# Kernel optimization log

Hardware: AMD Instinct MI355X
Metric: run time of the kernel (lower is better)

Reference implementation:

```python
import jax, jax.numpy as jnp
import numpy as np

B, S, D = 8, 4096, 64
NEG = 10000.0


def setup_inputs() -> dict:
    key = jax.random.key(0)
    k1, k2, k3, k4 = jax.random.split(key, 4)
    query = jax.random.normal(k1, (B, S, D), dtype=jnp.float32)
    k_ = jax.random.normal(k2, (B, S, D), dtype=jnp.float32)
    v_ = jax.random.normal(k3, (B, S, D), dtype=jnp.float32)
    # padding mask [B, Sk]: mostly valid, tail padded for some rows
    lens = jax.random.randint(k4, (B,), S // 2, S + 1)
    mask = jnp.arange(S)[None, :] < lens[:, None]
    return {"query": query, "key": k_, "value": v_, "mask": mask}


def reference(query, key, value, mask):
    d = query.shape[-1]
    scale = 1.0 / jnp.sqrt(jnp.asarray(d, dtype=query.dtype))
    # e: [B, Sq, Sk]
    e = jnp.einsum("bqd,bkd->bqk", query, key) * scale
    # causal (history_only) mask: key index > query index gets -10000
    q_idx = jnp.arange(query.shape[1])[:, None]
    k_idx = jnp.arange(key.shape[1])[None, :]
    e = e - NEG * (k_idx > q_idx).astype(e.dtype)[None, :, :]
    # padding mask [B, 1, Sk]
    e = e - NEG * (1.0 - mask.astype(e.dtype))[:, None, :]
    attention = jax.nn.softmax(e, axis=-1)
    return jnp.einsum("bqk,bkd->bqd", attention, value)
```

## Files before the change

kernel.cpp:

```cpp
#include <hip/hip_runtime.h>
#include <hip/hip_bf16.h>

#define B_N 8
#define S_N 4096
#define D_N 64
#define NQT 64
#define TILE_BYTES 8192
#define SLOT_BYTES 4352

typedef __attribute__((ext_vector_type(8))) short bf16x8;
typedef __attribute__((ext_vector_type(4))) float f32x4;
typedef __attribute__((ext_vector_type(16))) float f32x16;
typedef unsigned uint2v __attribute__((ext_vector_type(2)));
typedef unsigned uint4v __attribute__((ext_vector_type(4)));

__device__ __forceinline__ float fast_exp2(float x) {
#if __has_builtin(__builtin_amdgcn_exp2f)
  return __builtin_amdgcn_exp2f(x);
#else
  return exp2f(x);
#endif
}

__device__ __forceinline__ unsigned f2bf_u(float x) {
  __hip_bfloat16 h = __float2bfloat16(x);
  return (unsigned)__builtin_bit_cast(unsigned short, h);
}
__device__ __forceinline__ unsigned pack2(float a, float b) {
  return f2bf_u(a) | (f2bf_u(b) << 16);
}

__device__ __forceinline__ void pl32swap(unsigned& a, unsigned& b) {
#if __has_builtin(__builtin_amdgcn_permlane32_swap)
  uint2v r = __builtin_amdgcn_permlane32_swap(a, b, false, false);
  a = r[0];
  b = r[1];
#else
  asm volatile("v_permlane32_swap_b32 %0, %1" : "+v"(a), "+v"(b));
#endif
}
__device__ __forceinline__ float xhalf_sum(float x) {
  unsigned a = __builtin_bit_cast(unsigned, x), b = a;
  pl32swap(a, b);
  return __builtin_bit_cast(float, a) + __builtin_bit_cast(float, b);
}

__global__ void __launch_bounds__(256)
lens_kernel(const unsigned* __restrict__ mask, int* __restrict__ lens) {
  int b = blockIdx.x, tid = threadIdx.x;
  unsigned first = mask[0];
  int cnt = 0;
  if (first == 0x01010101u) {
    const unsigned char* m = ((const unsigned char*)mask) + (size_t)b * S_N;
    for (int i = tid; i < S_N; i += 256) cnt += (m[i] != 0);
  } else if (first == 0x3F800000u) {
    const float* m = ((const float*)mask) + (size_t)b * S_N;
    for (int i = tid; i < S_N; i += 256) cnt += (m[i] != 0.0f);
  } else {
    const int* m = ((const int*)mask) + (size_t)b * S_N;
    for (int i = tid; i < S_N; i += 256) cnt += (m[i] != 0);
  }
#pragma unroll
  for (int off = 32; off > 0; off >>= 1) cnt += __shfl_down(cnt, off);
  __shared__ int acc[4];
  if ((tid & 63) == 0) acc[tid >> 6] = cnt;
  __syncthreads();
  if (tid == 0) lens[b] = acc[0] + acc[1] + acc[2] + acc[3];
}

__global__ void __launch_bounds__(256)
prep_kernel(const float* __restrict__ K, const float* __restrict__ V,
            char* __restrict__ Ks, char* __restrict__ VTs) {
  __shared__ float vl[64][72];
  const int bt = blockIdx.x, tid = threadIdx.x;
  const float* Kt = K + (size_t)bt * 4096;
  const float* Vt = V + (size_t)bt * 4096;
  char* Ko = Ks + (size_t)bt * TILE_BYTES;
  char* Vo = VTs + (size_t)bt * TILE_BYTES;
#pragma unroll
  for (int i = 0; i < 2; ++i) {
    int c = tid + i * 256;
    int r = c >> 3, j = c & 7;
    f32x4 a = *(const f32x4*)(Kt + r * 64 + j * 8);
    f32x4 b4 = *(const f32x4*)(Kt + r * 64 + j * 8 + 4);
    union { bf16x8 v; unsigned u[4]; } pk;
    pk.u[0] = pack2(a[0], a[1]);   pk.u[1] = pack2(a[2], a[3]);
    pk.u[2] = pack2(b4[0], b4[1]); pk.u[3] = pack2(b4[2], b4[3]);
    *(bf16x8*)(Ko + ((r >> 5) * 4 + (j >> 1)) * 1024 + (j & 1) * 512 +
               (r & 31) * 16) = pk.v;
    f32x4 va = *(const f32x4*)(Vt + r * 64 + j * 8);
    f32x4 vb = *(const f32x4*)(Vt + r * 64 + j * 8 + 4);
#pragma unroll
    for (int e = 0; e < 4; ++e) vl[j * 8 + e][r] = va[e];
#pragma unroll
    for (int e = 0; e < 4; ++e) vl[j * 8 + 4 + e][r] = vb[e];
  }
  __syncthreads();
#pragma unroll
  for (int i = 0; i < 2; ++i) {
    int c = tid + i * 256;
    int d = c >> 3, j = c & 7;
    f32x4 fa = *(const f32x4*)(&vl[d][j * 8]);
    f32x4 fb = *(const f32x4*)(&vl[d][j * 8 + 4]);
    union { bf16x8 v; unsigned u[4]; } pk;
    pk.u[0] = pack2(fa[0], fa[1]); pk.u[1] = pack2(fa[2], fa[3]);
    pk.u[2] = pack2(fb[0], fb[1]); pk.u[3] = pack2(fb[2], fb[3]);
    *(bf16x8*)(Vo + ((d >> 5) * 4 + (j >> 1)) * 1024 + (j & 1) * 512 +
               (d & 31) * 16) = pk.v;
  }
}

__global__ void __launch_bounds__(256, 4)
attn_kernel(const float* __restrict__ Qg, const char* __restrict__ Ks,
            const char* __restrict__ VTs, const int* __restrict__ lens,
            float* __restrict__ Og, char* __restrict__ parts,
            int M, int U) {
  const int tid = threadIdx.x;
  const int lane = tid & 63;
  const int w = tid >> 6;
  const int bid = blockIdx.x;
  const int b = bid & 7;
  const int u2 = (bid >> 3) * 4 + w;
  const int ws = u2 & 1;
  const int u = (U - 1) - (u2 >> 1);
  int a = 0;
  while ((M * (a + 1) * (a + 2)) / 2 <= u) ++a;
  const int v = u - (M * a * (a + 1)) / 2;
  const int qt = a * M + v / (a + 1);
  const int s = v - (v / (a + 1)) * (a + 1);
  const int kq = a + 1;

  const int q0 = qt * 64;
  const int len = lens[b];
  int nt = (len + 63) >> 6;
  if (qt + 1 < nt) nt = qt + 1;
  const int beg = s * M;
  int cnt = nt - beg;
  if (cnt > M) cnt = M;
  if (cnt < 0) cnt = 0;

  const int q31 = lane & 31;
  const int h = lane >> 5;
  const int qg = q0 + ws * 32 + q31;

  const char* Kb = Ks + (size_t)(b * NQT) * TILE_BYTES;
  const char* Vb = VTs + (size_t)(b * NQT) * TILE_BYTES;

  constexpr float CS = 0.125f * 1.4426950408889634f;
  bf16x8 qf[4];
#pragma unroll
  for (int c = 0; c < 4; ++c) {
    const float* src = Qg + ((size_t)(b * S_N) + qg) * D_N + c * 16 + h * 8;
    f32x4 aa = *(const f32x4*)src;
    f32x4 b4 = *(const f32x4*)(src + 4);
    union { bf16x8 v; unsigned u[4]; } pk;
    pk.u[0] = pack2(aa[0] * CS, aa[1] * CS);
    pk.u[1] = pack2(aa[2] * CS, aa[3] * CS);
    pk.u[2] = pack2(b4[0] * CS, b4[1] * CS);
    pk.u[3] = pack2(b4[2] * CS, b4[3] * CS);
    qf[c] = pk.v;
  }

  f32x16 ot0 = {}, ot1 = {};
  float l = 0.0f;
  const int H = 2 * cnt;

  for (int hs = 0; hs < H; ++hs) {
    const int t = beg + (hs >> 1);
    const int half = hs & 1;

    bf16x8 kd[4], vd[4];
    const char* Kt = Kb + (size_t)t * TILE_BYTES + half * 4096 + lane * 16;
    const char* Vt = Vb + (size_t)t * TILE_BYTES + half * 2048 + lane * 16;
#pragma unroll
    for (int c = 0; c < 4; ++c) kd[c] = *(const bf16x8*)(Kt + c * 1024);
    vd[0] = *(const bf16x8*)(Vt);
    vd[1] = *(const bf16x8*)(Vt + 1024);
    vd[2] = *(const bf16x8*)(Vt + 4096);
    vd[3] = *(const bf16x8*)(Vt + 5120);

    f32x16 sv;
#pragma unroll
    for (int i = 0; i < 16; ++i) sv[i] = -8.0f;
    __builtin_amdgcn_s_setprio(1);
#pragma unroll
    for (int c = 0; c < 4; ++c)
      sv = __builtin_amdgcn_mfma_f32_32x32x16_bf16(kd[c], qf[c], sv, 0, 0, 0);
    __builtin_amdgcn_s_setprio(0);

    const int kb0 = t * 64 + half * 32;
    if (t == qt || t * 64 + 64 > len) {
#pragma unroll
      for (int g = 0; g < 4; ++g)
#pragma unroll
        for (int jj = 0; jj < 4; ++jj) {
          int kg = kb0 + 8 * g + 4 * h + jj;
          if (kg > qg || kg >= len) sv[g * 4 + jj] = -10000.0f;
        }
    }

    float ps0 = 0.f, ps1 = 0.f, ps2 = 0.f, ps3 = 0.f;
#pragma unroll
    for (int g = 0; g < 4; ++g) {
      sv[4 * g + 0] = fast_exp2(sv[4 * g + 0]); ps0 += sv[4 * g + 0];
      sv[4 * g + 1] = fast_exp2(sv[4 * g + 1]); ps1 += sv[4 * g + 1];
      sv[4 * g + 2] = fast_exp2(sv[4 * g + 2]); ps2 += sv[4 * g + 2];
      sv[4 * g + 3] = fast_exp2(sv[4 * g + 3]); ps3 += sv[4 * g + 3];
    }
    l += xhalf_sum((ps0 + ps1) + (ps2 + ps3));

    unsigned opk[4][2];
#pragma unroll
    for (int g = 0; g < 4; ++g) {
      opk[g][0] = pack2(sv[4 * g + 0], sv[4 * g + 1]);
      opk[g][1] = pack2(sv[4 * g + 2], sv[4 * g + 3]);
    }
    bf16x8 pb2[2];
#pragma unroll
    for (int c2 = 0; c2 < 2; ++c2) {
      const int g0 = 2 * c2, g1 = g0 + 1;
      unsigned a0 = opk[g0][0], b0 = opk[g1][0];
      unsigned a1 = opk[g0][1], b1 = opk[g1][1];
      pl32swap(a0, b0);
      pl32swap(a1, b1);
      union { bf16x8 v; unsigned u[4]; } pk;
      pk.u[0] = a0; pk.u[1] = a1; pk.u[2] = b0; pk.u[3] = b1;
      pb2[c2] = pk.v;
    }

    __builtin_amdgcn_s_setprio(1);
    ot0 = __builtin_amdgcn_mfma_f32_32x32x16_bf16(vd[0], pb2[0], ot0, 0, 0, 0);
    ot0 = __builtin_amdgcn_mfma_f32_32x32x16_bf16(vd[1], pb2[1], ot0, 0, 0, 0);
    ot1 = __builtin_amdgcn_mfma_f32_32x32x16_bf16(vd[2], pb2[0], ot1, 0, 0, 0);
    ot1 = __builtin_amdgcn_mfma_f32_32x32x16_bf16(vd[3], pb2[1], ot1, 0, 0, 0);
    __builtin_amdgcn_s_setprio(0);
  }

  if (kq == 1) {
    float linv = 1.0f / l;
    float* orow = Og + ((size_t)(b * S_N) + qg) * D_N;
#pragma unroll
    for (int g = 0; g < 4; ++g) {
      f32x4 oa = {ot0[4 * g + 0] * linv, ot0[4 * g + 1] * linv,
                  ot0[4 * g + 2] * linv, ot0[4 * g + 3] * linv};
      *(f32x4*)(orow + 8 * g + 4 * h) = oa;
      f32x4 ob = {ot1[4 * g + 0] * linv, ot1[4 * g + 1] * linv,
                  ot1[4 * g + 2] * linv, ot1[4 * g + 3] * linv};
      *(f32x4*)(orow + 32 + 8 * g + 4 * h) = ob;
    }
  } else {
    char* slot = parts + (((size_t)b * U + u) * 2 + ws) * SLOT_BYTES;
    unsigned wv[16];
#pragma unroll
    for (int jj = 0; jj < 8; ++jj) {
      wv[jj] = pack2(ot0[2 * jj], ot0[2 * jj + 1]);
      wv[8 + jj] = pack2(ot1[2 * jj], ot1[2 * jj + 1]);
    }
    uint4v* dst = (uint4v*)(slot + lane * 64);
#pragma unroll
    for (int q4 = 0; q4 < 4; ++q4)
      dst[q4] = (uint4v){wv[4 * q4], wv[4 * q4 + 1], wv[4 * q4 + 2], wv[4 * q4 + 3]};
    *(float*)(slot + 4096 + lane * 4) = l;
  }
}

__global__ void __launch_bounds__(128)
merge_kernel(const char* __restrict__ parts, float* __restrict__ Og,
             int M, int U) {
  const int bid = blockIdx.x;
  const int b = bid & 7, qt = bid >> 3;
  const int a = qt / M;
  const int kq = a + 1;
  if (kq == 1) return;
  const int tid = threadIdx.x;
  const int ws = tid >> 6;
  const int lane = tid & 63;
  const int base_u = (M * a * (a + 1)) / 2 + (qt - a * M) * (a + 1);

  float acc[32];
#pragma unroll
  for (int i = 0; i < 32; ++i) acc[i] = 0.0f;
  float L = 0.0f;
  for (int s2 = 0; s2 < kq; ++s2) {
    const char* slot =
        parts + (((size_t)b * U + base_u + s2) * 2 + ws) * SLOT_BYTES;
    const uint4v* src = (const uint4v*)(slot + lane * 64);
#pragma unroll
    for (int q4 = 0; q4 < 4; ++q4) {
      uint4v wv = src[q4];
#pragma unroll
      for (int e = 0; e < 4; ++e) {
        unsigned uw = wv[e];
        acc[2 * (4 * q4 + e)] += __builtin_bit_cast(float, uw << 16);
        acc[2 * (4 * q4 + e) + 1] += __builtin_bit_cast(float, uw & 0xFFFF0000u);
      }
    }
    L += *(const float*)(slot + 4096 + lane * 4);
  }
  float linv = 1.0f / L;
  const int q31 = lane & 31;
  const int h = lane >> 5;
  float* orow = Og + ((size_t)(b * S_N) + qt * 64 + ws * 32 + q31) * D_N;
#pragma unroll
  for (int dt = 0; dt < 2; ++dt)
#pragma unroll
    for (int g = 0; g < 4; ++g) {
      f32x4 w = {acc[dt * 16 + 4 * g + 0] * linv, acc[dt * 16 + 4 * g + 1] * linv,
                 acc[dt * 16 + 4 * g + 2] * linv, acc[dt * 16 + 4 * g + 3] * linv};
      *(f32x4*)(orow + dt * 32 + 8 * g + 4 * h) = w;
    }
}

extern "C" void kernel_launch(void* const* d_in, const int* in_sizes, int n_in,
                              void* d_out, int out_size, void* d_ws, size_t ws_size,
                              hipStream_t stream) {
  const float* Qg = (const float*)d_in[0];
  const float* Kg = (const float*)d_in[1];
  const float* Vg = (const float*)d_in[2];
  const unsigned* mask = (const unsigned*)d_in[3];
  float* Og = (float*)d_out;

  int* lens = (int*)d_ws;
  char* Ks = (char*)d_ws + 4096;
  char* VTs = Ks + (size_t)B_N * NQT * TILE_BYTES;
  char* parts = VTs + (size_t)B_N * NQT * TILE_BYTES;

  int M = 8, U = 288;
  size_t need = 4096 + ((size_t)2 * B_N * NQT * TILE_BYTES) +
                (size_t)B_N * 288 * 2 * SLOT_BYTES;
  if (ws_size < need) { M = 64; U = 64; }

  lens_kernel<<<dim3(B_N), dim3(256), 0, stream>>>(mask, lens);
  prep_kernel<<<dim3(B_N * NQT), dim3(256), 0, stream>>>(Kg, Vg, Ks, VTs);
  attn_kernel<<<dim3(B_N * U / 2), dim3(256), 0, stream>>>(Qg, Ks, VTs, lens,
                                                           Og, parts, M, U);
  if (M == 8)
    merge_kernel<<<dim3(B_N * NQT), dim3(128), 0, stream>>>(parts, Og, M, U);
}
```

Baseline: 57.66 us.

## Double-buffer K/V tiles per wave via async global-to-LDS loads

Each wave now prefetches the next half-tile of K and V into its own LDS double buffer with global_load_lds, then reads the current tile from LDS instead of loading straight from global memory into registers. The aim is to hide global load latency behind the MFMA and softmax work of the current step. The cost is 64KB of shared memory per block, which can lower occupancy below the declared 4 blocks per CU, plus manual waitcnt sequencing that must stay correct.

```diff
diff --git a/kernel.cpp b/kernel.cpp
--- a/kernel.cpp
+++ b/kernel.cpp
@@ -44,6 +44,11 @@
   pl32swap(a, b);
   return __builtin_bit_cast(float, a) + __builtin_bit_cast(float, b);
 }
+
+#define GLOAD(g, l)                                                  \
+  __builtin_amdgcn_global_load_lds(                                  \
+      (const __attribute__((address_space(1))) unsigned*)(g),        \
+      (__attribute__((address_space(3))) unsigned*)(l), 16, 0, 0)
 
 __global__ void __launch_bounds__(256)
 lens_kernel(const unsigned* __restrict__ mask, int* __restrict__ lens) {
@@ -115,6 +120,7 @@
             const char* __restrict__ VTs, const int* __restrict__ lens,
             float* __restrict__ Og, char* __restrict__ parts,
             int M, int U) {
+  __shared__ __align__(16) char sm[65536];
   const int tid = threadIdx.x;
   const int lane = tid & 63;
   const int w = tid >> 6;
@@ -145,6 +151,22 @@
 
   const char* Kb = Ks + (size_t)(b * NQT) * TILE_BYTES;
   const char* Vb = VTs + (size_t)(b * NQT) * TILE_BYTES;
+  char* lbase = sm + w * 16384;
+
+  auto issue = [&](int hs2) __attribute__((always_inline)) {
+    const int t = beg + (hs2 >> 1);
+    const int half = hs2 & 1;
+    const char* Kt = Kb + (size_t)t * TILE_BYTES + half * 4096 + lane * 16;
+    const char* Vt = Vb + (size_t)t * TILE_BYTES + half * 2048 + lane * 16;
+    char* kd = lbase + (hs2 & 1) * 8192;
+    char* vd = kd + 4096;
+#pragma unroll
+    for (int c = 0; c < 4; ++c) GLOAD(Kt + c * 1024, kd + c * 1024);
+    GLOAD(Vt, vd);
+    GLOAD(Vt + 1024, vd + 1024);
+    GLOAD(Vt + 4096, vd + 2048);
+    GLOAD(Vt + 5120, vd + 3072);
+  };
 
   constexpr float CS = 0.125f * 1.4426950408889634f;
   bf16x8 qf[4];
@@ -165,19 +187,30 @@
   float l = 0.0f;
   const int H = 2 * cnt;
 
+  if (H > 0) issue(0);
+
   for (int hs = 0; hs < H; ++hs) {
     const int t = beg + (hs >> 1);
     const int half = hs & 1;
 
+    asm volatile("s_waitcnt lgkmcnt(0)" ::: "memory");
+    __builtin_amdgcn_sched_barrier(0);
+    if (hs + 1 < H) {
+      issue(hs + 1);
+      __builtin_amdgcn_sched_barrier(0);
+      asm volatile("s_waitcnt vmcnt(8)" ::: "memory");
+    } else {
+      asm volatile("s_waitcnt vmcnt(0)" ::: "memory");
+    }
+    __builtin_amdgcn_sched_barrier(0);
+
+    const char* kl = lbase + (hs & 1) * 8192 + lane * 16;
     bf16x8 kd[4], vd[4];
-    const char* Kt = Kb + (size_t)t * TILE_BYTES + half * 4096 + lane * 16;
-    const char* Vt = Vb + (size_t)t * TILE_BYTES + half * 2048 + lane * 16;
-#pragma unroll
-    for (int c = 0; c < 4; ++c) kd[c] = *(const bf16x8*)(Kt + c * 1024);
-    vd[0] = *(const bf16x8*)(Vt);
-    vd[1] = *(const bf16x8*)(Vt + 1024);
-    vd[2] = *(const bf16x8*)(Vt + 4096);
-    vd[3] = *(const bf16x8*)(Vt + 5120);
+#pragma unroll
+    for (int c = 0; c < 4; ++c) {
+      kd[c] = *(const bf16x8*)(kl + c * 1024);
+      vd[c] = *(const bf16x8*)(kl + 4096 + c * 1024);
+    }
 
     f32x16 sv;
 #pragma unroll
```

Result: slower. 70.58 us (+22.4%).
